# Kernel tuning notes

Measured on AMD Instinct MI355X. Metric: run time of the kernel, lower is better.

Reference implementation:

```python
import jax, jax.numpy as jnp
import numpy as np

HEADS = 4
WS = 8
EPS = 1e-6


def setup_inputs() -> dict:
    key = jax.random.key(0)
    k1, k2, k3 = jax.random.split(key, 3)
    B, C, H, W = 8, 128, 256, 256
    x = jax.random.normal(k1, (B, C, H, W), dtype=jnp.float32)
    norm_w = jnp.ones((C,), dtype=jnp.float32)
    norm_b = jnp.zeros((C,), dtype=jnp.float32)
    qkv_w = jax.random.normal(k2, (3 * C, C), dtype=jnp.float32) * (C ** -0.5)
    qkv_b = jnp.zeros((3 * C,), dtype=jnp.float32)
    proj_w = jax.random.normal(k3, (C, C), dtype=jnp.float32) * (C ** -0.5)
    proj_b = jnp.zeros((C,), dtype=jnp.float32)
    return {"x": x, "norm_w": norm_w, "norm_b": norm_b,
            "qkv_w": qkv_w, "qkv_b": qkv_b,
            "proj_w": proj_w, "proj_b": proj_b}


def reference(x, norm_w, norm_b, qkv_w, qkv_b, proj_w, proj_b):
    B, C, H, W = x.shape
    heads, ws = HEADS, WS
    d = C // heads
    Nh, Nw = H // ws, W // ws
    scale = d ** -0.5

    # LayerNorm2d: normalize over spatial dims (H, W) per (B, C)
    mean = x.mean(axis=(2, 3), keepdims=True)
    var = x.var(axis=(2, 3), keepdims=True)  # ddof=0 == unbiased=False
    xn = (x - mean) / jnp.sqrt(var + EPS)
    xn = norm_w[None, :, None, None] * xn + norm_b[None, :, None, None]

    # 1x1 conv == channel matmul
    qkv = jnp.einsum('oc,bchw->bohw', qkv_w, xn) + qkv_b[None, :, None, None]
    q, k, v = jnp.split(qkv, 3, axis=1)

    def window(t):
        # b (h d) (Nh ws1) (Nw ws2) -> b Nh Nw h (ws1 ws2) d
        t = t.reshape(B, heads, d, Nh, ws, Nw, ws)
        t = t.transpose(0, 3, 5, 1, 4, 6, 2)
        return t.reshape(B, Nh, Nw, heads, ws * ws, d)

    qw, kw, vw = window(q), window(k), window(v)

    attn = jax.nn.softmax(jnp.einsum('...qd,...kd->...qk', qw, kw) * scale, axis=-1)
    out = jnp.einsum('...qk,...kd->...qd', attn, vw)

    # b Nh Nw h (ws1 ws2) d -> b (h d) (Nh ws1) (Nw ws2)
    out = out.reshape(B, Nh, Nw, heads, ws, ws, d)
    out = out.transpose(0, 3, 6, 1, 4, 2, 5).reshape(B, C, H, W)

    out = jnp.einsum('oc,bchw->bohw', proj_w, out) + proj_b[None, :, None, None]
    return out
```

## Files before the change

kernel.cpp:

```cpp
#include <hip/hip_runtime.h>
#include <hip/hip_bf16.h>

#define C_    128
#define HW_   65536
#define B_    8
#define WIMG_ 256

typedef __attribute__((ext_vector_type(8))) short short8;
typedef __attribute__((ext_vector_type(4))) short short4b;
typedef __attribute__((ext_vector_type(4))) float floatx4;

static __device__ __forceinline__ short f2bf(float x) {
  __hip_bfloat16 h = __float2bfloat16(x);
  return *reinterpret_cast<short*>(&h);
}
static __device__ __forceinline__ int pack2(float a, float b) {
  return (int)(unsigned short)f2bf(a) | ((int)(unsigned short)f2bf(b) << 16);
}

__global__ __launch_bounds__(1024) void ln_stats_kernel(const float* __restrict__ x,
                                                        float* __restrict__ stats) {
  const int bc = ((blockIdx.x & 7) << 7) + (blockIdx.x >> 3);
  const float4* p4 = (const float4*)(x + (size_t)bc * HW_);
  float4 v[16];
  #pragma unroll
  for (int k = 0; k < 16; ++k) v[k] = p4[threadIdx.x + (k << 10)];
  float s = 0.f, ss = 0.f;
  #pragma unroll
  for (int k = 0; k < 16; ++k) {
    s  += (v[k].x + v[k].y) + (v[k].z + v[k].w);
    ss += (v[k].x * v[k].x + v[k].y * v[k].y) + (v[k].z * v[k].z + v[k].w * v[k].w);
  }
  #pragma unroll
  for (int off = 32; off > 0; off >>= 1) {
    s  += __shfl_down(s, off, 64);
    ss += __shfl_down(ss, off, 64);
  }
  __shared__ float red[32];
  const int wv = threadIdx.x >> 6;
  if ((threadIdx.x & 63) == 0) { red[wv * 2] = s; red[wv * 2 + 1] = ss; }
  __syncthreads();
  if (threadIdx.x == 0) {
    float S = 0.f, SS = 0.f;
    #pragma unroll
    for (int v2 = 0; v2 < 16; ++v2) { S += red[v2 * 2]; SS += red[v2 * 2 + 1]; }
    const float mean = S * (1.f / HW_);
    const float var  = SS * (1.f / HW_) - mean * mean;
    stats[bc * 2]     = mean;
    stats[bc * 2 + 1] = rsqrtf(var + 1e-6f);
  }
}

__global__ __launch_bounds__(256) void cvt_w_kernel(const float* __restrict__ qkv_w,
                                                    const float* __restrict__ proj_w,
                                                    short* __restrict__ dst) {
  const int i = blockIdx.x * 256 + threadIdx.x;
  float v = (i < 49152) ? qkv_w[i] : proj_w[i - 49152];
  if (i < 16384) v *= 0.17677669529663687f;
  dst[i] = f2bf(v);
}

__global__ __launch_bounds__(256, 3) void win_attn_kernel(
    const float* __restrict__ x, const float* __restrict__ stats,
    const float* __restrict__ norm_w, const float* __restrict__ norm_b,
    const short* __restrict__ wq, const float* __restrict__ qkv_b,
    const short* __restrict__ wp, const float* __restrict__ proj_b,
    float* __restrict__ out)
{
  __shared__ __align__(16) char lds[53248];
  short* Xn = (short*)lds;
  short* Qr = (short*)lds;
  short* Kr = (short*)(lds + 17408);
  short* Vr = (short*)(lds + 34816);

  const int tid = threadIdx.x;
  const int l15 = tid & 15;
  const int qd  = (tid >> 4) & 3;
  const int w   = tid >> 6;

  const int bid = blockIdx.x;
  const int W   = ((bid & 7) << 10) + (bid >> 3);
  const int ww  = W & 31;
  const int wh  = (W >> 5) & 31;
  const int b   = W >> 10;

  const float* xb = x + (size_t)b * C_ * HW_ + (size_t)(wh * 8) * WIMG_ + ww * 8;
  const float* st = stats + b * C_ * 2;

  {
    const int c = tid >> 1, half = tid & 1;
    const float aa = st[c * 2 + 1] * norm_w[c];
    const float bb = norm_b[c] - st[c * 2] * aa;
    const float* xc = xb + (size_t)c * HW_ + half * 4;
    float4 v[8];
    #pragma unroll
    for (int r = 0; r < 8; ++r) v[r] = *(const float4*)(xc + r * WIMG_);
    #pragma unroll
    for (int r = 0; r < 8; ++r) {
      const int t = r * 8 + half * 4;
      Xn[(t + 0) * 136 + c] = f2bf(v[r].x * aa + bb);
      Xn[(t + 1) * 136 + c] = f2bf(v[r].y * aa + bb);
      Xn[(t + 2) * 136 + c] = f2bf(v[r].z * aa + bb);
      Xn[(t + 3) * 136 + c] = f2bf(v[r].w * aa + bb);
    }
  }
  __syncthreads();

  const float scale = 0.17677669529663687f;

  floatx4 acc[6][4];
  const int ro = w * 96;
  {
    #pragma unroll
    for (int mt = 0; mt < 6; ++mt) {
      const bool isq = (ro + mt * 16) < 128;
      #pragma unroll
      for (int r = 0; r < 4; ++r) {
        float bias = qkv_b[ro + mt * 16 + qd * 4 + r];
        if (isq) bias *= scale;
        #pragma unroll
        for (int nt = 0; nt < 4; ++nt) acc[mt][nt][r] = bias;
      }
    }
    #pragma unroll
    for (int kb = 0; kb < 4; ++kb) {
      short8 bfr[4];
      #pragma unroll
      for (int nt = 0; nt < 4; ++nt)
        bfr[nt] = *(const short8*)&Xn[(nt * 16 + l15) * 136 + kb * 32 + qd * 8];
      #pragma unroll
      for (int mt = 0; mt < 6; ++mt) {
        short8 af = *(const short8*)&wq[(ro + mt * 16 + l15) * 128 + kb * 32 + qd * 8];
        #pragma unroll
        for (int nt = 0; nt < 4; ++nt)
          acc[mt][nt] = __builtin_amdgcn_mfma_f32_16x16x32_bf16(af, bfr[nt], acc[mt][nt], 0, 0, 0);
      }
    }
  }
  __syncthreads();

  {
    #pragma unroll
    for (int mt = 0; mt < 6; ++mt) {
      const int ob = ro + mt * 16;
      #pragma unroll
      for (int nt = 0; nt < 4; ++nt) {
        const int t = nt * 16 + l15;
        floatx4 a = acc[mt][nt];
        if (ob < 128) {
          const int ol = ob + qd * 4;
          *(int*)&Qr[t * 136 + ol]     = pack2(a[0], a[1]);
          *(int*)&Qr[t * 136 + ol + 2] = pack2(a[2], a[3]);
        } else if (ob < 256) {
          const int ol = (ob - 128) + qd * 4;
          *(int*)&Kr[t * 136 + ol]     = pack2(a[0], a[1]);
          *(int*)&Kr[t * 136 + ol + 2] = pack2(a[2], a[3]);
        } else {
          const int o0 = (ob - 256) + qd * 4;
          #pragma unroll
          for (int r = 0; r < 4; ++r) Vr[(o0 + r) * 72 + t] = f2bf(a[r]);
        }
      }
    }
  }
  __syncthreads();

  const int h = w;
  floatx4 s[4][4];
  {
    short8 qa[4], ka[4];
    #pragma unroll
    for (int it = 0; it < 4; ++it)
      qa[it] = *(const short8*)&Qr[(it * 16 + l15) * 136 + h * 32 + qd * 8];
    #pragma unroll
    for (int jt = 0; jt < 4; ++jt)
      ka[jt] = *(const short8*)&Kr[(jt * 16 + l15) * 136 + h * 32 + qd * 8];
    const floatx4 z = {0.f, 0.f, 0.f, 0.f};
    #pragma unroll
    for (int it = 0; it < 4; ++it)
      #pragma unroll
      for (int jt = 0; jt < 4; ++jt)
        s[it][jt] = __builtin_amdgcn_mfma_f32_16x16x32_bf16(qa[it], ka[jt], z, 0, 0, 0);
  }
  float rs[4][4];
  #pragma unroll
  for (int it = 0; it < 4; ++it)
    #pragma unroll
    for (int r = 0; r < 4; ++r) {
      float m = fmaxf(fmaxf(s[it][0][r], s[it][1][r]), fmaxf(s[it][2][r], s[it][3][r]));
      m = fmaxf(m, __shfl_xor(m, 1)); m = fmaxf(m, __shfl_xor(m, 2));
      m = fmaxf(m, __shfl_xor(m, 4)); m = fmaxf(m, __shfl_xor(m, 8));
      float sm = 0.f;
      #pragma unroll
      for (int jt = 0; jt < 4; ++jt) { s[it][jt][r] = __expf(s[it][jt][r] - m); sm += s[it][jt][r]; }
      sm += __shfl_xor(sm, 1); sm += __shfl_xor(sm, 2);
      sm += __shfl_xor(sm, 4); sm += __shfl_xor(sm, 8);
      rs[it][r] = 1.f / sm;
    }
  __syncthreads();

  short* Pw = (short*)(lds + w * 8704);
  #pragma unroll
  for (int it = 0; it < 4; ++it)
    #pragma unroll
    for (int jt = 0; jt < 4; ++jt)
      #pragma unroll
      for (int r = 0; r < 4; ++r)
        Pw[(it * 16 + qd * 4 + r) * 68 + jt * 16 + l15] = f2bf(s[it][jt][r]);
  __syncthreads();

  floatx4 o[4][2];
  #pragma unroll
  for (int it = 0; it < 4; ++it)
    #pragma unroll
    for (int dt = 0; dt < 2; ++dt) o[it][dt] = (floatx4){0.f, 0.f, 0.f, 0.f};
  #pragma unroll
  for (int kb = 0; kb < 2; ++kb) {
    short8 pa[4], vb[2];
    #pragma unroll
    for (int it = 0; it < 4; ++it) {
      short4b plo = *(const short4b*)&Pw[(it * 16 + l15) * 68 + kb * 32 + qd * 8];
      short4b phi = *(const short4b*)&Pw[(it * 16 + l15) * 68 + kb * 32 + qd * 8 + 4];
      pa[it] = __builtin_shufflevector(plo, phi, 0, 1, 2, 3, 4, 5, 6, 7);
    }
    #pragma unroll
    for (int dt = 0; dt < 2; ++dt)
      vb[dt] = *(const short8*)&Vr[(h * 32 + dt * 16 + l15) * 72 + kb * 32 + qd * 8];
    #pragma unroll
    for (int it = 0; it < 4; ++it)
      #pragma unroll
      for (int dt = 0; dt < 2; ++dt)
        o[it][dt] = __builtin_amdgcn_mfma_f32_16x16x32_bf16(pa[it], vb[dt], o[it][dt], 0, 0, 0);
  }
  __syncthreads();

  short* Att = (short*)lds;
  #pragma unroll
  for (int it = 0; it < 4; ++it)
    #pragma unroll
    for (int dt = 0; dt < 2; ++dt)
      #pragma unroll
      for (int r = 0; r < 4; ++r)
        Att[(it * 16 + qd * 4 + r) * 136 + h * 32 + dt * 16 + l15] = f2bf(o[it][dt][r] * rs[it][r]);
  __syncthreads();

  {
    floatx4 pacc[2][4];
    #pragma unroll
    for (int mt = 0; mt < 2; ++mt)
      #pragma unroll
      for (int r = 0; r < 4; ++r) {
        const float bias = proj_b[w * 32 + mt * 16 + qd * 4 + r];
        #pragma unroll
        for (int nt = 0; nt < 4; ++nt) pacc[mt][nt][r] = bias;
      }
    #pragma unroll
    for (int kb = 0; kb < 4; ++kb) {
      short8 bfr[4];
      #pragma unroll
      for (int nt = 0; nt < 4; ++nt)
        bfr[nt] = *(const short8*)&Att[(nt * 16 + l15) * 136 + kb * 32 + qd * 8];
      #pragma unroll
      for (int mt = 0; mt < 2; ++mt) {
        short8 af = *(const short8*)&wp[(w * 32 + mt * 16 + l15) * 128 + kb * 32 + qd * 8];
        #pragma unroll
        for (int nt = 0; nt < 4; ++nt)
          pacc[mt][nt] = __builtin_amdgcn_mfma_f32_16x16x32_bf16(af, bfr[nt], pacc[mt][nt], 0, 0, 0);
      }
    }
    float* ob_ = out + (size_t)b * C_ * HW_ + (size_t)(wh * 8) * WIMG_ + ww * 8;
    #pragma unroll
    for (int mt = 0; mt < 2; ++mt)
      #pragma unroll
      for (int nt = 0; nt < 4; ++nt)
        #pragma unroll
        for (int r = 0; r < 4; ++r) {
          const int oc = w * 32 + mt * 16 + qd * 4 + r;
          const int t  = nt * 16 + l15;
          ob_[(size_t)oc * HW_ + (t >> 3) * WIMG_ + (t & 7)] = pacc[mt][nt][r];
        }
  }
}

extern "C" void kernel_launch(void* const* d_in, const int* in_sizes, int n_in,
                              void* d_out, int out_size, void* d_ws, size_t ws_size,
                              hipStream_t stream) {
  const float* x      = (const float*)d_in[0];
  const float* norm_w = (const float*)d_in[1];
  const float* norm_b = (const float*)d_in[2];
  const float* qkv_w  = (const float*)d_in[3];
  const float* qkv_b  = (const float*)d_in[4];
  const float* proj_w = (const float*)d_in[5];
  const float* proj_b = (const float*)d_in[6];
  float* out   = (float*)d_out;
  float* stats = (float*)d_ws;
  short* wq    = (short*)((char*)d_ws + 8192);
  short* wp    = wq + 384 * 128;

  hipLaunchKernelGGL(cvt_w_kernel, dim3(256), dim3(256), 0, stream, qkv_w, proj_w, wq);
  hipLaunchKernelGGL(ln_stats_kernel, dim3(B_ * C_), dim3(1024), 0, stream, x, stats);
  hipLaunchKernelGGL(win_attn_kernel, dim3(32 * 32 * B_), dim3(256), 0, stream,
                     x, stats, norm_w, norm_b, wq, qkv_b, wp, proj_b, out);
}
```

Baseline: 716.4 us.

## Split LN stats into partial+final passes, use DPP softmax and exp2, reshape QK LDS

The LayerNorm statistics pass is split into 8192 small blocks that write partial sums, plus a tiny final reduction kernel, to raise parallelism over the single 1024-thread block per channel. The softmax reductions now use DPP row operations instead of shuffles, and exp2 is used with log2(e) folded into the Q weight scale. Q and K are interleaved in one LDS buffer with stride 272, and P is written into the consumed Q/K columns, which removes two barriers and the split short4 loads. In exchange there is one more kernel launch and a more intricate LDS aliasing scheme that relies on each wave writing only into the columns it has already read.

```diff
diff --git a/kernel.cpp b/kernel.cpp
--- a/kernel.cpp
+++ b/kernel.cpp
@@ -7,7 +7,6 @@
 #define WIMG_ 256
 
 typedef __attribute__((ext_vector_type(8))) short short8;
-typedef __attribute__((ext_vector_type(4))) short short4b;
 typedef __attribute__((ext_vector_type(4))) float floatx4;
 
 static __device__ __forceinline__ short f2bf(float x) {
@@ -18,16 +17,27 @@
   return (int)(unsigned short)f2bf(a) | ((int)(unsigned short)f2bf(b) << 16);
 }
 
-__global__ __launch_bounds__(1024) void ln_stats_kernel(const float* __restrict__ x,
-                                                        float* __restrict__ stats) {
-  const int bc = ((blockIdx.x & 7) << 7) + (blockIdx.x >> 3);
-  const float4* p4 = (const float4*)(x + (size_t)bc * HW_);
-  float4 v[16];
-  #pragma unroll
-  for (int k = 0; k < 16; ++k) v[k] = p4[threadIdx.x + (k << 10)];
+template<int CTRL>
+static __device__ __forceinline__ float fmax_dpp(float x) {
+  int p = __builtin_amdgcn_update_dpp(0, __builtin_bit_cast(int, x), CTRL, 0xF, 0xF, true);
+  return fmaxf(x, __builtin_bit_cast(float, p));
+}
+template<int CTRL>
+static __device__ __forceinline__ float fadd_dpp(float x) {
+  int p = __builtin_amdgcn_update_dpp(0, __builtin_bit_cast(int, x), CTRL, 0xF, 0xF, true);
+  return x + __builtin_bit_cast(float, p);
+}
+
+__global__ __launch_bounds__(256) void ln_part_kernel(const float* __restrict__ x,
+                                                      float2* __restrict__ part) {
+  const int cid = ((blockIdx.x & 7) << 10) | (blockIdx.x >> 3);
+  const float4* p4 = (const float4*)(x + (size_t)cid * 8192);
+  float4 v[8];
+  #pragma unroll
+  for (int k = 0; k < 8; ++k) v[k] = p4[threadIdx.x + (k << 8)];
   float s = 0.f, ss = 0.f;
   #pragma unroll
-  for (int k = 0; k < 16; ++k) {
+  for (int k = 0; k < 8; ++k) {
     s  += (v[k].x + v[k].y) + (v[k].z + v[k].w);
     ss += (v[k].x * v[k].x + v[k].y * v[k].y) + (v[k].z * v[k].z + v[k].w * v[k].w);
   }
@@ -36,19 +46,27 @@
     s  += __shfl_down(s, off, 64);
     ss += __shfl_down(ss, off, 64);
   }
-  __shared__ float red[32];
+  __shared__ float red[8];
   const int wv = threadIdx.x >> 6;
   if ((threadIdx.x & 63) == 0) { red[wv * 2] = s; red[wv * 2 + 1] = ss; }
   __syncthreads();
   if (threadIdx.x == 0) {
-    float S = 0.f, SS = 0.f;
-    #pragma unroll
-    for (int v2 = 0; v2 < 16; ++v2) { S += red[v2 * 2]; SS += red[v2 * 2 + 1]; }
-    const float mean = S * (1.f / HW_);
-    const float var  = SS * (1.f / HW_) - mean * mean;
-    stats[bc * 2]     = mean;
-    stats[bc * 2 + 1] = rsqrtf(var + 1e-6f);
-  }
+    float S = red[0] + red[2] + red[4] + red[6];
+    float SS = red[1] + red[3] + red[5] + red[7];
+    part[cid] = make_float2(S, SS);
+  }
+}
+
+__global__ __launch_bounds__(256) void ln_final_kernel(const float2* __restrict__ part,
+                                                       float* __restrict__ stats) {
+  const int bc = blockIdx.x * 256 + threadIdx.x;
+  float S = 0.f, SS = 0.f;
+  #pragma unroll
+  for (int k = 0; k < 8; ++k) { float2 p = part[bc * 8 + k]; S += p.x; SS += p.y; }
+  const float mean = S * (1.f / HW_);
+  const float var  = SS * (1.f / HW_) - mean * mean;
+  stats[bc * 2]     = mean;
+  stats[bc * 2 + 1] = rsqrtf(var + 1e-6f);
 }
 
 __global__ __launch_bounds__(256) void cvt_w_kernel(const float* __restrict__ qkv_w,
@@ -56,7 +74,7 @@
                                                     short* __restrict__ dst) {
   const int i = blockIdx.x * 256 + threadIdx.x;
   float v = (i < 49152) ? qkv_w[i] : proj_w[i - 49152];
-  if (i < 16384) v *= 0.17677669529663687f;
+  if (i < 16384) v *= 0.17677669529663687f * 1.4426950408889634f;
   dst[i] = f2bf(v);
 }
 
@@ -69,8 +87,7 @@
 {
   __shared__ __align__(16) char lds[53248];
   short* Xn = (short*)lds;
-  short* Qr = (short*)lds;
-  short* Kr = (short*)(lds + 17408);
+  short* QK = (short*)lds;
   short* Vr = (short*)(lds + 34816);
 
   const int tid = threadIdx.x;
@@ -106,8 +123,6 @@
   }
   __syncthreads();
 
-  const float scale = 0.17677669529663687f;
-
   floatx4 acc[6][4];
   const int ro = w * 96;
   {
@@ -117,7 +132,7 @@
       #pragma unroll
       for (int r = 0; r < 4; ++r) {
         float bias = qkv_b[ro + mt * 16 + qd * 4 + r];
-        if (isq) bias *= scale;
+        if (isq) bias *= 0.17677669529663687f * 1.4426950408889634f;
         #pragma unroll
         for (int nt = 0; nt < 4; ++nt) acc[mt][nt][r] = bias;
       }
@@ -149,12 +164,12 @@
         floatx4 a = acc[mt][nt];
         if (ob < 128) {
           const int ol = ob + qd * 4;
-          *(int*)&Qr[t * 136 + ol]     = pack2(a[0], a[1]);
-          *(int*)&Qr[t * 136 + ol + 2] = pack2(a[2], a[3]);
+          *(int*)&QK[t * 272 + ol]     = pack2(a[0], a[1]);
+          *(int*)&QK[t * 272 + ol + 2] = pack2(a[2], a[3]);
         } else if (ob < 256) {
-          const int ol = (ob - 128) + qd * 4;
-          *(int*)&Kr[t * 136 + ol]     = pack2(a[0], a[1]);
-          *(int*)&Kr[t * 136 + ol + 2] = pack2(a[2], a[3]);
+          const int ol = 136 + (ob - 128) + qd * 4;
+          *(int*)&QK[t * 272 + ol]     = pack2(a[0], a[1]);
+          *(int*)&QK[t * 272 + ol + 2] = pack2(a[2], a[3]);
         } else {
           const int o0 = (ob - 256) + qd * 4;
           #pragma unroll
@@ -171,10 +186,10 @@
     short8 qa[4], ka[4];
     #pragma unroll
     for (int it = 0; it < 4; ++it)
-      qa[it] = *(const short8*)&Qr[(it * 16 + l15) * 136 + h * 32 + qd * 8];
+      qa[it] = *(const short8*)&QK[(it * 16 + l15) * 272 + h * 32 + qd * 8];
     #pragma unroll
     for (int jt = 0; jt < 4; ++jt)
-      ka[jt] = *(const short8*)&Kr[(jt * 16 + l15) * 136 + h * 32 + qd * 8];
+      ka[jt] = *(const short8*)&QK[(jt * 16 + l15) * 272 + 136 + h * 32 + qd * 8];
     const floatx4 z = {0.f, 0.f, 0.f, 0.f};
     #pragma unroll
     for (int it = 0; it < 4; ++it)
@@ -188,26 +203,28 @@
     #pragma unroll
     for (int r = 0; r < 4; ++r) {
       float m = fmaxf(fmaxf(s[it][0][r], s[it][1][r]), fmaxf(s[it][2][r], s[it][3][r]));
-      m = fmaxf(m, __shfl_xor(m, 1)); m = fmaxf(m, __shfl_xor(m, 2));
-      m = fmaxf(m, __shfl_xor(m, 4)); m = fmaxf(m, __shfl_xor(m, 8));
+      m = fmax_dpp<0x128>(m); m = fmax_dpp<0x124>(m);
+      m = fmax_dpp<0x122>(m); m = fmax_dpp<0x121>(m);
       float sm = 0.f;
       #pragma unroll
-      for (int jt = 0; jt < 4; ++jt) { s[it][jt][r] = __expf(s[it][jt][r] - m); sm += s[it][jt][r]; }
-      sm += __shfl_xor(sm, 1); sm += __shfl_xor(sm, 2);
-      sm += __shfl_xor(sm, 4); sm += __shfl_xor(sm, 8);
+      for (int jt = 0; jt < 4; ++jt) {
+        s[it][jt][r] = __builtin_amdgcn_exp2f(s[it][jt][r] - m);
+        sm += s[it][jt][r];
+      }
+      sm = fadd_dpp<0x128>(sm); sm = fadd_dpp<0x124>(sm);
+      sm = fadd_dpp<0x122>(sm); sm = fadd_dpp<0x121>(sm);
       rs[it][r] = 1.f / sm;
     }
-  __syncthreads();
-
-  short* Pw = (short*)(lds + w * 8704);
+
   #pragma unroll
   for (int it = 0; it < 4; ++it)
     #pragma unroll
-    for (int jt = 0; jt < 4; ++jt)
+    for (int jt = 0; jt < 4; ++jt) {
+      const int col = ((jt < 2) ? (w * 32 + jt * 16) : (104 + w * 32 + jt * 16)) + l15;
       #pragma unroll
       for (int r = 0; r < 4; ++r)
-        Pw[(it * 16 + qd * 4 + r) * 68 + jt * 16 + l15] = f2bf(s[it][jt][r]);
-  __syncthreads();
+        QK[(it * 16 + qd * 4 + r) * 272 + col] = f2bf(s[it][jt][r]);
+    }
 
   floatx4 o[4][2];
   #pragma unroll
@@ -216,13 +233,11 @@
     for (int dt = 0; dt < 2; ++dt) o[it][dt] = (floatx4){0.f, 0.f, 0.f, 0.f};
   #pragma unroll
   for (int kb = 0; kb < 2; ++kb) {
+    const int pcol = (kb == 0) ? (w * 32 + qd * 8) : (136 + w * 32 + qd * 8);
     short8 pa[4], vb[2];
     #pragma unroll
-    for (int it = 0; it < 4; ++it) {
-      short4b plo = *(const short4b*)&Pw[(it * 16 + l15) * 68 + kb * 32 + qd * 8];
-      short4b phi = *(const short4b*)&Pw[(it * 16 + l15) * 68 + kb * 32 + qd * 8 + 4];
-      pa[it] = __builtin_shufflevector(plo, phi, 0, 1, 2, 3, 4, 5, 6, 7);
-    }
+    for (int it = 0; it < 4; ++it)
+      pa[it] = *(const short8*)&QK[(it * 16 + l15) * 272 + pcol];
     #pragma unroll
     for (int dt = 0; dt < 2; ++dt)
       vb[dt] = *(const short8*)&Vr[(h * 32 + dt * 16 + l15) * 72 + kb * 32 + qd * 8];
@@ -296,9 +311,11 @@
   float* stats = (float*)d_ws;
   short* wq    = (short*)((char*)d_ws + 8192);
   short* wp    = wq + 384 * 128;
+  float2* part = (float2*)((char*)d_ws + 139264);
 
   hipLaunchKernelGGL(cvt_w_kernel, dim3(256), dim3(256), 0, stream, qkv_w, proj_w, wq);
-  hipLaunchKernelGGL(ln_stats_kernel, dim3(B_ * C_), dim3(1024), 0, stream, x, stats);
+  hipLaunchKernelGGL(ln_part_kernel, dim3(8192), dim3(256), 0, stream, x, part);
+  hipLaunchKernelGGL(ln_final_kernel, dim3(4), dim3(256), 0, stream, part, stats);
   hipLaunchKernelGGL(win_attn_kernel, dim3(32 * 32 * B_), dim3(256), 0, stream,
                      x, stats, norm_w, norm_b, wq, qkv_b, wp, proj_b, out);
 }
```

Measured after the change: 673.2 us. 6.0% less time.
